# Kernel tuning notes

Measured on AMD Instinct MI355X. Metric: run time of the kernel, lower is better.

## Reference

```python
import jax, jax.numpy as jnp
import numpy as np

N_NODES = 100000
N_EDGES = 1600000
IN_CH = 64
HID = 64
OUT_CH = 128
EDGE_CH = 3
OBS_RANGE = 0.5
ATK_RANGE = 0.3


def setup_inputs() -> dict:
    key = jax.random.key(0)
    k = jax.random.split(key, 8)
    # node features: first column is an integer node type in {0,1,2}
    node_type = jax.random.randint(k[0], (N_NODES, 1), 0, 3).astype(jnp.float32)
    feats = jax.random.normal(k[1], (N_NODES, IN_CH - 1), dtype=jnp.float32)
    x = jnp.concatenate([node_type, feats], axis=-1)
    edge_index = jax.random.randint(k[2], (2, N_EDGES), 0, N_NODES)
    # edge_attr[:,0] = distance in [0,1)
    edge_attr = jax.random.uniform(k[3], (N_EDGES, EDGE_CH), dtype=jnp.float32)
    s1 = 1.0 / np.sqrt(2 * IN_CH + EDGE_CH)
    s2 = 1.0 / np.sqrt(HID)
    W1 = jax.random.normal(k[4], (2 * IN_CH + EDGE_CH, HID), dtype=jnp.float32) * s1
    b1 = jnp.zeros((HID,), dtype=jnp.float32)
    W2 = jax.random.normal(k[5], (HID, OUT_CH), dtype=jnp.float32) * s2
    b2 = jnp.zeros((OUT_CH,), dtype=jnp.float32)
    return {"x": x, "edge_index": edge_index, "edge_attr": edge_attr,
            "W1": W1, "b1": b1, "W2": W2, "b2": b2}


def reference(x, edge_index, edge_attr, W1, b1, W2, b2):
    src = edge_index[0]  # j (source)
    dst = edge_index[1]  # i (target)
    x_j = x[src]         # [E, IN_CH]
    x_i = x[dst]         # [E, IN_CH]
    h = jnp.concatenate([x_i, x_j, edge_attr], axis=-1)  # [E, 2*IN_CH+3]
    msg = jax.nn.relu(h @ W1 + b1) @ W2 + b2             # [E, OUT_CH]
    dist = edge_attr[:, 0]
    ntype = x_j[:, 0]
    mask = jnp.where(ntype == 0, dist < OBS_RANGE,
                     jnp.where(ntype == 1, dist < ATK_RANGE, True))
    msg = mask[:, None].astype(msg.dtype) * msg
    out = jax.ops.segment_sum(msg, dst, num_segments=x.shape[0])  # [N, OUT_CH]
    return jax.nn.relu(out)
```

## Files before the change

### kernel.cpp

```cpp
#include <hip/hip_runtime.h>

#define N_NODES 100000
#define N_EDGES 1600000
#define IN_CH   64
#define HID_CH  64
#define OUT_CH  128

typedef __attribute__((ext_vector_type(8))) __bf16    bf16x8;
typedef __attribute__((ext_vector_type(4))) float     f32x4;
typedef __attribute__((ext_vector_type(2))) _Float16  f16x2;
typedef __attribute__((ext_vector_type(8))) _Float16  f16x8;

#define OFF_HSUM   0
#define OFF_XB     12800000
#define OFF_Z      25600000
#define OFF_CNT    51200000
#define OFF_NTYPE  51600000

__device__ __forceinline__ unsigned short f2bf(float f) {
    union { float f; unsigned int i; } c;
    c.f = f;
    unsigned int u = c.i;
    unsigned int r = (u + 0x7FFFu + ((u >> 16) & 1u)) >> 16;
    return (unsigned short)r;
}

__device__ __forceinline__ void atomic_pk_add_f16(unsigned int* addr, f16x2 val) {
    typedef __attribute__((address_space(1))) f16x2 gf16x2;
    __builtin_amdgcn_global_atomic_fadd_v2f16((gf16x2*)(void*)addr, val);
}

__global__ void gnn_prep(const float* __restrict__ xf,
                         unsigned short* __restrict__ xb,
                         unsigned char* __restrict__ ntype,
                         uint4* __restrict__ hz,
                         float4* __restrict__ cz) {
    int i = blockIdx.x * blockDim.x + threadIdx.x;
    if (i < 1600000) {
        float4 v = reinterpret_cast<const float4*>(xf)[i];
        ushort4 o;
        o.x = f2bf(v.x); o.y = f2bf(v.y); o.z = f2bf(v.z); o.w = f2bf(v.w);
        reinterpret_cast<ushort4*>(xb)[i] = o;
        if ((i & 15) == 0) {
            int n = i >> 4;
            ntype[n] = (v.x == 0.0f) ? 0 : ((v.x == 1.0f) ? 1 : 2);
        }
    } else if (i < 2400000) {
        hz[i - 1600000] = (uint4){0u, 0u, 0u, 0u};
    } else if (i < 2425000) {
        cz[i - 2400000] = (float4){0.f, 0.f, 0.f, 0.f};
    }
}

__global__ __launch_bounds__(256, 4) void gnn_zgemm(
    const unsigned short* __restrict__ xb,
    const float*          __restrict__ W1,
    _Float16*             __restrict__ z)
{
    __shared__ __align__(16) unsigned short BT[128][72];

    const int tid  = threadIdx.x;
    const int wave = tid >> 6;
    const int lane = tid & 63;
    const int q    = lane >> 4;
    const int m16  = lane & 15;

    for (int idx = tid; idx < 64 * 128; idx += 256) {
        int k = idx >> 7, j = idx & 127;
        BT[j][k] = f2bf(W1[(k + ((j >= 64) ? 64 : 0)) * 64 + (j & 63)]);
    }
    __syncthreads();

    const int nodeBase = (blockIdx.x * 4 + wave) * 32;
    if (nodeBase >= N_NODES) return;

    f32x4 acc[2][8];
#pragma unroll
    for (int mt = 0; mt < 2; ++mt)
#pragma unroll
        for (int nt = 0; nt < 8; ++nt)
            acc[mt][nt] = (f32x4){0.0f, 0.0f, 0.0f, 0.0f};

#pragma unroll
    for (int kc = 0; kc < 2; ++kc) {
        bf16x8 af[2];
#pragma unroll
        for (int mt = 0; mt < 2; ++mt) {
            int node = nodeBase + mt * 16 + m16;
            if (node >= N_NODES) node = N_NODES - 1;
            af[mt] = *reinterpret_cast<const bf16x8*>(
                xb + (size_t)node * IN_CH + kc * 32 + q * 8);
        }
#pragma unroll
        for (int nt = 0; nt < 8; ++nt) {
            bf16x8 bfr = *reinterpret_cast<const bf16x8*>(
                &BT[nt * 16 + m16][kc * 32 + q * 8]);
            acc[0][nt] = __builtin_amdgcn_mfma_f32_16x16x32_bf16(af[0], bfr, acc[0][nt], 0, 0, 0);
            acc[1][nt] = __builtin_amdgcn_mfma_f32_16x16x32_bf16(af[1], bfr, acc[1][nt], 0, 0, 0);
        }
    }

#pragma unroll
    for (int mt = 0; mt < 2; ++mt) {
#pragma unroll
        for (int nt = 0; nt < 8; ++nt) {
            int col = nt * 16 + m16;
#pragma unroll
            for (int r = 0; r < 4; ++r) {
                int n = nodeBase + mt * 16 + q * 4 + r;
                if (n < N_NODES)
                    z[(size_t)n * 128 + col] = (_Float16)acc[mt][nt][r];
            }
        }
    }
}

__global__ __launch_bounds__(256, 4) void gnn_edge_quad(
    const int*           __restrict__ eidx,
    const float*         __restrict__ ea,
    const unsigned char* __restrict__ ntype,
    const _Float16*      __restrict__ z,
    const float*         __restrict__ W1,
    const float*         __restrict__ b1,
    unsigned int*        __restrict__ hsum,
    float*               __restrict__ cnt)
{
    const int tid  = threadIdx.x;
    const int lane = tid & 63;
    const int q    = lane >> 4;
    const int m16  = lane & 15;

    const int c0 = 2 * m16;
    const float wx0 = W1[128 * 64 + c0],      wx1 = W1[128 * 64 + c0 + 1];
    const float wx2 = W1[128 * 64 + c0 + 32], wx3 = W1[128 * 64 + c0 + 33];
    const float wy0 = W1[129 * 64 + c0],      wy1 = W1[129 * 64 + c0 + 1];
    const float wy2 = W1[129 * 64 + c0 + 32], wy3 = W1[129 * 64 + c0 + 33];
    const float wz0 = W1[130 * 64 + c0],      wz1 = W1[130 * 64 + c0 + 1];
    const float wz2 = W1[130 * 64 + c0 + 32], wz3 = W1[130 * 64 + c0 + 33];
    const float bb0 = b1[c0],                 bb1 = b1[c0 + 1];
    const float bb2 = b1[c0 + 32],            bb3 = b1[c0 + 33];

    const int wid    = (blockIdx.x * 256 + tid) >> 6;
    const int nwaves = (gridDim.x * 256) >> 6;

    for (int e = wid * 4 + q; e < N_EDGES; e += nwaves * 4) {
        int   s  = eidx[e];
        float a0 = ea[e * 3 + 0];
        int ntc = ntype[s];
        bool mk = (ntc == 0) ? (a0 < 0.5f) : ((ntc == 1) ? (a0 < 0.3f) : true);
        if (!mk) continue;

        int   d  = eidx[N_EDGES + e];
        float a1 = ea[e * 3 + 1];
        float a2 = ea[e * 3 + 2];

        const _Float16* zd = z + (size_t)d * 128;
        const _Float16* zs = z + (size_t)s * 128 + 64;
        f16x2 zd01 = *reinterpret_cast<const f16x2*>(zd + c0);
        f16x2 zd23 = *reinterpret_cast<const f16x2*>(zd + c0 + 32);
        f16x2 zs01 = *reinterpret_cast<const f16x2*>(zs + c0);
        f16x2 zs23 = *reinterpret_cast<const f16x2*>(zs + c0 + 32);

        float h0 = (float)zd01[0] + (float)zs01[0] + bb0 + a0 * wx0 + a1 * wy0 + a2 * wz0;
        float h1 = (float)zd01[1] + (float)zs01[1] + bb1 + a0 * wx1 + a1 * wy1 + a2 * wz1;
        float h2 = (float)zd23[0] + (float)zs23[0] + bb2 + a0 * wx2 + a1 * wy2 + a2 * wz2;
        float h3 = (float)zd23[1] + (float)zs23[1] + bb3 + a0 * wx3 + a1 * wy3 + a2 * wz3;
        h0 = h0 > 0.f ? h0 : 0.f;
        h1 = h1 > 0.f ? h1 : 0.f;
        h2 = h2 > 0.f ? h2 : 0.f;
        h3 = h3 > 0.f ? h3 : 0.f;

        unsigned int* hb = hsum + (size_t)d * 32;
        if (h0 + h1 > 0.f) {
            f16x2 pk = {(_Float16)h0, (_Float16)h1};
            atomic_pk_add_f16(hb + m16, pk);
        }
        if (h2 + h3 > 0.f) {
            f16x2 pk = {(_Float16)h2, (_Float16)h3};
            atomic_pk_add_f16(hb + 16 + m16, pk);
        }
        if (m16 == 0) unsafeAtomicAdd(&cnt[d], 1.0f);
    }
}

__global__ __launch_bounds__(256, 4) void gnn_node_out(
    const _Float16* __restrict__ hsum,
    const float*    __restrict__ cnt,
    const float*    __restrict__ W2,
    const float*    __restrict__ b2,
    float*          __restrict__ out)
{
    __shared__ __align__(16) unsigned short W2T[128][72];
    __shared__ float b2s[128];

    const int tid  = threadIdx.x;
    const int wave = tid >> 6;
    const int lane = tid & 63;
    const int q    = lane >> 4;
    const int m16  = lane & 15;

    const int nodeBase = (blockIdx.x * 4 + wave) * 32;

    f16x8 hpre[2][2];
    float cc[2][4];
#pragma unroll
    for (int kc = 0; kc < 2; ++kc)
#pragma unroll
        for (int mt = 0; mt < 2; ++mt) {
            int node = nodeBase + mt * 16 + m16;
            if (node >= N_NODES) node = N_NODES - 1;
            hpre[kc][mt] = *reinterpret_cast<const f16x8*>(
                hsum + (size_t)node * HID_CH + kc * 32 + q * 8);
        }
#pragma unroll
    for (int mt = 0; mt < 2; ++mt)
#pragma unroll
        for (int r = 0; r < 4; ++r) {
            int n = nodeBase + mt * 16 + q * 4 + r;
            cc[mt][r] = (n < N_NODES) ? cnt[n] : 0.0f;
        }

    for (int idx = tid; idx < 64 * 128; idx += 256) {
        int k = idx >> 7, n = idx & 127;
        W2T[n][k] = f2bf(W2[k * 128 + n]);
    }
    if (tid < 128) b2s[tid] = b2[tid];
    __syncthreads();

    if (nodeBase >= N_NODES) return;

    f32x4 acc[2][8];
#pragma unroll
    for (int mt = 0; mt < 2; ++mt)
#pragma unroll
        for (int nt = 0; nt < 8; ++nt)
            acc[mt][nt] = (f32x4){0.0f, 0.0f, 0.0f, 0.0f};

#pragma unroll
    for (int kc = 0; kc < 2; ++kc) {
        bf16x8 af[2];
#pragma unroll
        for (int mt = 0; mt < 2; ++mt) {
            union { bf16x8 v; unsigned short u[8]; } rr;
#pragma unroll
            for (int j = 0; j < 8; ++j) rr.u[j] = f2bf((float)hpre[kc][mt][j]);
            af[mt] = rr.v;
        }
#pragma unroll
        for (int nt = 0; nt < 8; ++nt) {
            bf16x8 bfr = *reinterpret_cast<const bf16x8*>(
                &W2T[nt * 16 + m16][kc * 32 + q * 8]);
            acc[0][nt] = __builtin_amdgcn_mfma_f32_16x16x32_bf16(af[0], bfr, acc[0][nt], 0, 0, 0);
            acc[1][nt] = __builtin_amdgcn_mfma_f32_16x16x32_bf16(af[1], bfr, acc[1][nt], 0, 0, 0);
        }
    }

#pragma unroll
    for (int mt = 0; mt < 2; ++mt) {
        int nn[4];
#pragma unroll
        for (int r = 0; r < 4; ++r)
            nn[r] = nodeBase + mt * 16 + q * 4 + r;
#pragma unroll
        for (int nt = 0; nt < 8; ++nt) {
            int col = nt * 16 + m16;
            float bb = b2s[col];
#pragma unroll
            for (int r = 0; r < 4; ++r) {
                if (nn[r] < N_NODES) {
                    float v = acc[mt][nt][r] + cc[mt][r] * bb;
                    out[(size_t)nn[r] * OUT_CH + col] = v > 0.0f ? v : 0.0f;
                }
            }
        }
    }
}

extern "C" void kernel_launch(void* const* d_in, const int* in_sizes, int n_in,
                              void* d_out, int out_size, void* d_ws, size_t ws_size,
                              hipStream_t stream) {
    const float* x  = (const float*)d_in[0];
    const int*   ei = (const int*)d_in[1];
    const float* ea = (const float*)d_in[2];
    const float* W1 = (const float*)d_in[3];
    const float* b1 = (const float*)d_in[4];
    const float* W2 = (const float*)d_in[5];
    const float* b2 = (const float*)d_in[6];
    float* out = (float*)d_out;

    char* wsb = (char*)d_ws;
    unsigned int*   hsum  = (unsigned int*)  (wsb + OFF_HSUM);
    unsigned short* xb    = (unsigned short*)(wsb + OFF_XB);
    _Float16*       z     = (_Float16*)      (wsb + OFF_Z);
    float*          cnt   = (float*)         (wsb + OFF_CNT);
    unsigned char*  ntype = (unsigned char*) (wsb + OFF_NTYPE);

    gnn_prep<<<(2425000 + 255) / 256, 256, 0, stream>>>(
        x, xb, ntype, (uint4*)hsum, (float4*)cnt);

    gnn_zgemm<<<(N_NODES + 127) / 128, 256, 0, stream>>>(xb, W1, z);

    gnn_edge_quad<<<2048, 256, 0, stream>>>(ei, ea, ntype, z, W1, b1, hsum, cnt);

    gnn_node_out<<<(N_NODES + 127) / 128, 256, 0, stream>>>(
        (const _Float16*)hsum, cnt, W2, b2, out);
}
```

Baseline: 297.9 us.

## Compact masked edges into packed records and batch gathers per quad

A new compaction kernel evaluates the edge mask once per edge. It uses a wave ballot plus one atomic per wave to append surviving edges as 16-byte records (src, dst, dist, and two fp16 attributes) and accumulates the degree counts there. The edge kernel then walks only the dense record list, four edges per 16-lane group, and issues all z gathers before the arithmetic to raise memory-level parallelism and avoid divergent skipped edges. The bf16 conversion and node-type extraction move into the GEMM kernel, which removes the separate xb buffer pass. The trade-offs are an extra record write and read, fp16 rounding of two edge attributes, and a fixed record capacity sized near the expected survivor count, so edges beyond it would be silently dropped and the count would overrun.

```diff
diff --git a/kernel.cpp b/kernel.cpp
--- a/kernel.cpp
+++ b/kernel.cpp
@@ -12,10 +12,12 @@
 typedef __attribute__((ext_vector_type(8))) _Float16  f16x8;
 
 #define OFF_HSUM   0
-#define OFF_XB     12800000
-#define OFF_Z      25600000
-#define OFF_CNT    51200000
-#define OFF_NTYPE  51600000
+#define OFF_Z      12800000
+#define OFF_CREC   38400000
+#define OFF_CNT    54080000
+#define OFF_NTYPE  54480000
+#define OFF_CURSOR 54580000
+#define CREC_CAP   980000
 
 __device__ __forceinline__ unsigned short f2bf(float f) {
     union { float f; unsigned int i; } c;
@@ -30,32 +32,24 @@
     __builtin_amdgcn_global_atomic_fadd_v2f16((gf16x2*)(void*)addr, val);
 }
 
-__global__ void gnn_prep(const float* __restrict__ xf,
-                         unsigned short* __restrict__ xb,
-                         unsigned char* __restrict__ ntype,
-                         uint4* __restrict__ hz,
-                         float4* __restrict__ cz) {
+__global__ void gnn_prep0(uint4* __restrict__ hz,
+                          float4* __restrict__ cz,
+                          unsigned* __restrict__ cursor) {
     int i = blockIdx.x * blockDim.x + threadIdx.x;
-    if (i < 1600000) {
-        float4 v = reinterpret_cast<const float4*>(xf)[i];
-        ushort4 o;
-        o.x = f2bf(v.x); o.y = f2bf(v.y); o.z = f2bf(v.z); o.w = f2bf(v.w);
-        reinterpret_cast<ushort4*>(xb)[i] = o;
-        if ((i & 15) == 0) {
-            int n = i >> 4;
-            ntype[n] = (v.x == 0.0f) ? 0 : ((v.x == 1.0f) ? 1 : 2);
-        }
-    } else if (i < 2400000) {
-        hz[i - 1600000] = (uint4){0u, 0u, 0u, 0u};
-    } else if (i < 2425000) {
-        cz[i - 2400000] = (float4){0.f, 0.f, 0.f, 0.f};
+    if (i < 800000) {
+        hz[i] = (uint4){0u, 0u, 0u, 0u};
+    } else if (i < 825000) {
+        cz[i - 800000] = (float4){0.f, 0.f, 0.f, 0.f};
+    } else if (i == 825000) {
+        *cursor = 0u;
     }
 }
 
 __global__ __launch_bounds__(256, 4) void gnn_zgemm(
-    const unsigned short* __restrict__ xb,
-    const float*          __restrict__ W1,
-    _Float16*             __restrict__ z)
+    const float* __restrict__ x,
+    const float* __restrict__ W1,
+    _Float16*    __restrict__ z,
+    unsigned char* __restrict__ ntype)
 {
     __shared__ __align__(16) unsigned short BT[128][72];
 
@@ -88,8 +82,17 @@
         for (int mt = 0; mt < 2; ++mt) {
             int node = nodeBase + mt * 16 + m16;
             if (node >= N_NODES) node = N_NODES - 1;
-            af[mt] = *reinterpret_cast<const bf16x8*>(
-                xb + (size_t)node * IN_CH + kc * 32 + q * 8);
+            const float4* xr = reinterpret_cast<const float4*>(
+                x + (size_t)node * 64 + kc * 32 + q * 8);
+            float4 xa = xr[0], xb = xr[1];
+            union { bf16x8 v; unsigned short u[8]; } rr;
+            rr.u[0] = f2bf(xa.x); rr.u[1] = f2bf(xa.y);
+            rr.u[2] = f2bf(xa.z); rr.u[3] = f2bf(xa.w);
+            rr.u[4] = f2bf(xb.x); rr.u[5] = f2bf(xb.y);
+            rr.u[6] = f2bf(xb.z); rr.u[7] = f2bf(xb.w);
+            af[mt] = rr.v;
+            if (kc == 0 && q == 0)
+                ntype[node] = (xa.x == 0.0f) ? 0 : ((xa.x == 1.0f) ? 1 : 2);
         }
 #pragma unroll
         for (int nt = 0; nt < 8; ++nt) {
@@ -115,22 +118,58 @@
     }
 }
 
-__global__ __launch_bounds__(256, 4) void gnn_edge_quad(
-    const int*           __restrict__ eidx,
-    const float*         __restrict__ ea,
-    const unsigned char* __restrict__ ntype,
-    const _Float16*      __restrict__ z,
-    const float*         __restrict__ W1,
-    const float*         __restrict__ b1,
-    unsigned int*        __restrict__ hsum,
-    float*               __restrict__ cnt)
+__global__ void gnn_compact(const int* __restrict__ eidx,
+                            const float* __restrict__ ea,
+                            const unsigned char* __restrict__ ntype,
+                            unsigned* __restrict__ cursor,
+                            float4* __restrict__ crec,
+                            float* __restrict__ cnt) {
+    int e = blockIdx.x * 256 + threadIdx.x;
+    int lane = threadIdx.x & 63;
+
+    int s = eidx[e];
+    float a0 = ea[e * 3];
+    int ntc = ntype[s];
+    bool mk = (ntc == 0) ? (a0 < 0.5f) : ((ntc == 1) ? (a0 < 0.3f) : true);
+
+    unsigned long long bal = __ballot(mk);
+    int nact = __popcll(bal);
+    if (nact == 0) return;
+    int prefix = __popcll(bal & ((1ULL << lane) - 1ULL));
+    int leader = __ffsll((long long)bal) - 1;
+    unsigned base = 0;
+    if (lane == leader) base = atomicAdd(cursor, (unsigned)nact);
+    base = __shfl(base, leader);
+
+    if (mk) {
+        unsigned pos = base + (unsigned)prefix;
+        if (pos < CREC_CAP) {
+            int d = eidx[N_EDGES + e];
+            union { f16x2 v; float f; } pk;
+            pk.v = (f16x2){(_Float16)ea[e * 3 + 1], (_Float16)ea[e * 3 + 2]};
+            float4 rec;
+            rec.x = __int_as_float(s);
+            rec.y = __int_as_float(d);
+            rec.z = a0;
+            rec.w = pk.f;
+            crec[pos] = rec;
+            unsafeAtomicAdd(&cnt[d], 1.0f);
+        }
+    }
+}
+
+__global__ __launch_bounds__(256, 4) void gnn_edge_quad2(
+    const float4*   __restrict__ crec,
+    const unsigned* __restrict__ ncomp,
+    const _Float16* __restrict__ z,
+    const float*    __restrict__ W1,
+    const float*    __restrict__ b1,
+    unsigned int*   __restrict__ hsum)
 {
-    const int tid  = threadIdx.x;
-    const int lane = tid & 63;
-    const int q    = lane >> 4;
-    const int m16  = lane & 15;
-
-    const int c0 = 2 * m16;
+    const int tid = threadIdx.x;
+    const int m16 = tid & 15;
+    const int c0  = 2 * m16;
+
     const float wx0 = W1[128 * 64 + c0],      wx1 = W1[128 * 64 + c0 + 1];
     const float wx2 = W1[128 * 64 + c0 + 32], wx3 = W1[128 * 64 + c0 + 33];
     const float wy0 = W1[129 * 64 + c0],      wy1 = W1[129 * 64 + c0 + 1];
@@ -140,46 +179,61 @@
     const float bb0 = b1[c0],                 bb1 = b1[c0 + 1];
     const float bb2 = b1[c0 + 32],            bb3 = b1[c0 + 33];
 
-    const int wid    = (blockIdx.x * 256 + tid) >> 6;
-    const int nwaves = (gridDim.x * 256) >> 6;
-
-    for (int e = wid * 4 + q; e < N_EDGES; e += nwaves * 4) {
-        int   s  = eidx[e];
-        float a0 = ea[e * 3 + 0];
-        int ntc = ntype[s];
-        bool mk = (ntc == 0) ? (a0 < 0.5f) : ((ntc == 1) ? (a0 < 0.3f) : true);
-        if (!mk) continue;
-
-        int   d  = eidx[N_EDGES + e];
-        float a1 = ea[e * 3 + 1];
-        float a2 = ea[e * 3 + 2];
-
-        const _Float16* zd = z + (size_t)d * 128;
-        const _Float16* zs = z + (size_t)s * 128 + 64;
-        f16x2 zd01 = *reinterpret_cast<const f16x2*>(zd + c0);
-        f16x2 zd23 = *reinterpret_cast<const f16x2*>(zd + c0 + 32);
-        f16x2 zs01 = *reinterpret_cast<const f16x2*>(zs + c0);
-        f16x2 zs23 = *reinterpret_cast<const f16x2*>(zs + c0 + 32);
-
-        float h0 = (float)zd01[0] + (float)zs01[0] + bb0 + a0 * wx0 + a1 * wy0 + a2 * wz0;
-        float h1 = (float)zd01[1] + (float)zs01[1] + bb1 + a0 * wx1 + a1 * wy1 + a2 * wz1;
-        float h2 = (float)zd23[0] + (float)zs23[0] + bb2 + a0 * wx2 + a1 * wy2 + a2 * wz2;
-        float h3 = (float)zd23[1] + (float)zs23[1] + bb3 + a0 * wx3 + a1 * wy3 + a2 * wz3;
-        h0 = h0 > 0.f ? h0 : 0.f;
-        h1 = h1 > 0.f ? h1 : 0.f;
-        h2 = h2 > 0.f ? h2 : 0.f;
-        h3 = h3 > 0.f ? h3 : 0.f;
-
-        unsigned int* hb = hsum + (size_t)d * 32;
-        if (h0 + h1 > 0.f) {
-            f16x2 pk = {(_Float16)h0, (_Float16)h1};
-            atomic_pk_add_f16(hb + m16, pk);
-        }
-        if (h2 + h3 > 0.f) {
-            f16x2 pk = {(_Float16)h2, (_Float16)h3};
-            atomic_pk_add_f16(hb + 16 + m16, pk);
-        }
-        if (m16 == 0) unsafeAtomicAdd(&cnt[d], 1.0f);
+    const int n  = (int)*ncomp;
+    const int gq = (blockIdx.x * 256 + tid) >> 4;
+    const int nq = (gridDim.x * 256) >> 4;
+
+    for (int i0 = gq * 4; i0 < n; i0 += nq * 4) {
+        float4 rec[4];
+        bool   v[4];
+        int    s[4], d[4];
+#pragma unroll
+        for (int k = 0; k < 4; ++k) {
+            int i = i0 + k;
+            v[k] = (i < n);
+            rec[k] = v[k] ? crec[i] : (float4){0.f, 0.f, 0.f, 0.f};
+            s[k] = __float_as_int(rec[k].x);
+            d[k] = __float_as_int(rec[k].y);
+        }
+
+        f16x2 zd01[4], zd23[4], zs01[4], zs23[4];
+#pragma unroll
+        for (int k = 0; k < 4; ++k) {
+            const _Float16* zd = z + (size_t)d[k] * 128;
+            const _Float16* zs = z + (size_t)s[k] * 128 + 64;
+            zd01[k] = *reinterpret_cast<const f16x2*>(zd + c0);
+            zd23[k] = *reinterpret_cast<const f16x2*>(zd + c0 + 32);
+            zs01[k] = *reinterpret_cast<const f16x2*>(zs + c0);
+            zs23[k] = *reinterpret_cast<const f16x2*>(zs + c0 + 32);
+        }
+
+#pragma unroll
+        for (int k = 0; k < 4; ++k) {
+            if (!v[k]) continue;
+            float a0 = rec[k].z;
+            union { float f; f16x2 v2; } pk; pk.f = rec[k].w;
+            float a1 = (float)pk.v2[0];
+            float a2 = (float)pk.v2[1];
+
+            float h0 = (float)zd01[k][0] + (float)zs01[k][0] + bb0 + a0 * wx0 + a1 * wy0 + a2 * wz0;
+            float h1 = (float)zd01[k][1] + (float)zs01[k][1] + bb1 + a0 * wx1 + a1 * wy1 + a2 * wz1;
+            float h2 = (float)zd23[k][0] + (float)zs23[k][0] + bb2 + a0 * wx2 + a1 * wy2 + a2 * wz2;
+            float h3 = (float)zd23[k][1] + (float)zs23[k][1] + bb3 + a0 * wx3 + a1 * wy3 + a2 * wz3;
+            h0 = h0 > 0.f ? h0 : 0.f;
+            h1 = h1 > 0.f ? h1 : 0.f;
+            h2 = h2 > 0.f ? h2 : 0.f;
+            h3 = h3 > 0.f ? h3 : 0.f;
+
+            unsigned int* hb = hsum + (size_t)d[k] * 32;
+            if (h0 + h1 > 0.f) {
+                f16x2 p = {(_Float16)h0, (_Float16)h1};
+                atomic_pk_add_f16(hb + m16, p);
+            }
+            if (h2 + h3 > 0.f) {
+                f16x2 p = {(_Float16)h2, (_Float16)h3};
+                atomic_pk_add_f16(hb + 16 + m16, p);
+            }
+        }
     }
 }
 
@@ -289,18 +343,21 @@
     float* out = (float*)d_out;
 
     char* wsb = (char*)d_ws;
-    unsigned int*   hsum  = (unsigned int*)  (wsb + OFF_HSUM);
-    unsigned short* xb    = (unsigned short*)(wsb + OFF_XB);
-    _Float16*       z     = (_Float16*)      (wsb + OFF_Z);
-    float*          cnt   = (float*)         (wsb + OFF_CNT);
-    unsigned char*  ntype = (unsigned char*) (wsb + OFF_NTYPE);
-
-    gnn_prep<<<(2425000 + 255) / 256, 256, 0, stream>>>(
-        x, xb, ntype, (uint4*)hsum, (float4*)cnt);
-
-    gnn_zgemm<<<(N_NODES + 127) / 128, 256, 0, stream>>>(xb, W1, z);
-
-    gnn_edge_quad<<<2048, 256, 0, stream>>>(ei, ea, ntype, z, W1, b1, hsum, cnt);
+    unsigned int*   hsum   = (unsigned int*)  (wsb + OFF_HSUM);
+    _Float16*       z      = (_Float16*)      (wsb + OFF_Z);
+    float4*         crec   = (float4*)        (wsb + OFF_CREC);
+    float*          cnt    = (float*)         (wsb + OFF_CNT);
+    unsigned char*  ntype  = (unsigned char*) (wsb + OFF_NTYPE);
+    unsigned*       cursor = (unsigned*)      (wsb + OFF_CURSOR);
+
+    gnn_prep0<<<(825001 + 255) / 256, 256, 0, stream>>>(
+        (uint4*)hsum, (float4*)cnt, cursor);
+
+    gnn_zgemm<<<(N_NODES + 127) / 128, 256, 0, stream>>>(x, W1, z, ntype);
+
+    gnn_compact<<<N_EDGES / 256, 256, 0, stream>>>(ei, ea, ntype, cursor, crec, cnt);
+
+    gnn_edge_quad2<<<2048, 256, 0, stream>>>(crec, cursor, z, W1, b1, hsum);
 
     gnn_node_out<<<(N_NODES + 127) / 128, 256, 0, stream>>>(
         (const _Float16*)hsum, cnt, W2, b2, out);
```

Result: slower. 588.4 us (+97.5%).
